# Optimization experiments

Measured on AMD Instinct MI355X. Metric: run time of the kernel, lower is better.

The kernel has to match this reference:

```python
import jax, jax.numpy as jnp
import numpy as np

N_Q = 50000
BATCH = 512
SEQLEN = 500
MEM_SIZE = 64
DK = 128   # key_embedding_dim == key_memory_state_dim == final_fc_dim
DV = 256   # value_embedding_dim == value_memory_state_dim
FC = 128


def setup_inputs() -> dict:
    key = jax.random.key(0)
    ks = jax.random.split(key, 16)
    q_data = jax.random.randint(ks[0], (BATCH, SEQLEN), 0, N_Q + 1, dtype=jnp.int64)
    qa_data = jax.random.randint(ks[1], (BATCH, SEQLEN), 0, 2 * N_Q + 1, dtype=jnp.int64)
    u = jax.random.uniform(ks[2], (BATCH * SEQLEN, 1))
    target = jnp.where(u < 0.1, -1.0, jnp.round(jax.random.uniform(ks[3], (BATCH * SEQLEN, 1)))).astype(jnp.float32)
    # embedding tables with padding_idx=0 zeroed
    q_embed_W = (jax.random.normal(ks[4], (N_Q + 1, DK)) * (2.0 / DK) ** 0.5).at[0].set(0.0)
    qa_embed_W = (jax.random.normal(ks[5], (2 * N_Q + 1, DV)) * (2.0 / DV) ** 0.5).at[0].set(0.0)
    key_memory = jax.random.normal(ks[6], (MEM_SIZE, DK)) * (2.0 / DK) ** 0.5
    init_value_memory = jax.random.normal(ks[7], (MEM_SIZE, DV)) * (2.0 / DV) ** 0.5
    erase_W = jax.random.normal(ks[8], (DV, DV)) * (2.0 / DV) ** 0.5
    erase_b = jnp.zeros((DV,))
    add_W = jax.random.normal(ks[9], (DV, DV)) * (2.0 / DV) ** 0.5
    add_b = jnp.zeros((DV,))
    read_W = jax.random.normal(ks[10], (FC, DV + DK)) * (2.0 / (DV + DK)) ** 0.5
    read_b = jnp.zeros((FC,))
    pred_W = jax.random.normal(ks[11], (1, FC)) * (2.0 / FC) ** 0.5
    pred_b = jnp.zeros((1,))
    return dict(q_data=q_data, qa_data=qa_data, target=target,
                q_embed_W=q_embed_W, qa_embed_W=qa_embed_W,
                key_memory=key_memory, init_value_memory=init_value_memory,
                erase_W=erase_W, erase_b=erase_b, add_W=add_W, add_b=add_b,
                read_W=read_W, read_b=read_b, pred_W=pred_W, pred_b=pred_b)


def reference(q_data, qa_data, target, q_embed_W, qa_embed_W, key_memory,
              init_value_memory, erase_W, erase_b, add_W, add_b,
              read_W, read_b, pred_W, pred_b):
    B, S = q_data.shape
    q_e = q_embed_W[q_data]    # (B, S, DK)
    qa_e = qa_embed_W[qa_data]  # (B, S, DV)

    # Addressing weights do not depend on the value memory state -> batch them.
    cw = jax.nn.softmax(jnp.einsum('bsk,mk->bsm', q_e, key_memory), axis=-1)  # (B,S,M)
    erase = jax.nn.sigmoid(jnp.einsum('bsv,ev->bse', qa_e, erase_W) + erase_b)  # (B,S,DV)
    add = jnp.tanh(jnp.einsum('bsv,ev->bse', qa_e, add_W) + add_b)              # (B,S,DV)

    def step(mem, xs):
        w, er, ad = xs  # (B,M), (B,DV), (B,DV)
        read = jnp.einsum('bm,bmd->bd', w, mem)  # read before write
        mem = mem * (1.0 - w[:, :, None] * er[:, None, :]) + w[:, :, None] * ad[:, None, :]
        return mem, read

    init_mem = jnp.broadcast_to(init_value_memory, (B,) + init_value_memory.shape)
    _, reads = jax.lax.scan(step, init_mem,
                            (jnp.swapaxes(cw, 0, 1), jnp.swapaxes(erase, 0, 1), jnp.swapaxes(add, 0, 1)))
    reads = jnp.swapaxes(reads, 0, 1)  # (B, S, DV)

    predict_input = jnp.concatenate([reads, q_e], axis=-1).reshape(B * S, -1)
    h = jnp.tanh(predict_input @ read_W.T + read_b)
    logits = h @ pred_W.T + pred_b  # (B*S, 1)

    mask = target >= 0.0
    # numerically-stable BCE with logits
    bce = jnp.maximum(logits, 0.0) - logits * target + jnp.log1p(jnp.exp(-jnp.abs(logits)))
    denom = jnp.maximum(jnp.sum(mask.astype(logits.dtype)), 1.0)
    loss = jnp.sum(jnp.where(mask, bce, 0.0)) / denom
    # masked_select replaced by masked full-size outputs for static shapes
    pred_masked = jnp.where(mask, jax.nn.sigmoid(logits), 0.0)
    target_masked = jnp.where(mask, target, 0.0)
    return loss, pred_masked, target_masked
```

## Files before the change

### kernel.cpp

```cpp
#include <hip/hip_runtime.h>
#include <hip/hip_bf16.h>

#define BATCH 512
#define SEQ   500
#define BS    (BATCH*SEQ)
#define MEM   64
#define DK    128
#define DV    256
#define FC    128
#define KS    16

typedef float f32x4 __attribute__((ext_vector_type(4)));
typedef float f32x2 __attribute__((ext_vector_type(2)));
typedef unsigned int u32x4 __attribute__((ext_vector_type(4)));
typedef unsigned int u32x2 __attribute__((ext_vector_type(2)));
typedef unsigned short u16x8 __attribute__((ext_vector_type(8)));
typedef __bf16 bf16x8 __attribute__((ext_vector_type(8)));

__device__ __forceinline__ float bf2f(unsigned short u){ return __uint_as_float(((unsigned)u)<<16); }
__device__ __forceinline__ unsigned short f2bfu(float x){
  unsigned u = __float_as_uint(x);
  return (unsigned short)((u + 0x7FFFu + ((u>>16)&1u)) >> 16);
}
__device__ __forceinline__ float sigf(float x){ return 1.f/(1.f+__expf(-x)); }
__device__ __forceinline__ float tanh_fast(float x){ return 2.f/(1.f+__expf(-2.f*x)) - 1.f; }

#define DPP3(r) { \
  asm("v_add_f32_dpp %0, %0, %0 row_shr:1 row_mask:0xf bank_mask:0xf bound_ctrl:0" : "+v"(r)); \
  asm("v_add_f32_dpp %0, %0, %0 row_shr:2 row_mask:0xf bank_mask:0xf bound_ctrl:0" : "+v"(r)); \
  asm("v_add_f32_dpp %0, %0, %0 row_shr:4 row_mask:0xf bank_mask:0xf bound_ctrl:0" : "+v"(r)); \
}

__device__ __forceinline__ float ldF(const void* p, long i, int f32m){
  return f32m ? ((const float*)p)[i] : bf2f(((const unsigned short*)p)[i]);
}
__device__ __forceinline__ int ldI(const int* p, long i, int i64m){
  return i64m ? p[2*i] : p[i];
}
__device__ __forceinline__ void st8(unsigned short* dst, const void* src, long i, int f32m){
  if (f32m){
    const float* q = (const float*)src + i;
    f32x4 a = *(const f32x4*)q;
    f32x4 b = *(const f32x4*)(q+4);
    u16x8 o;
    o[0]=f2bfu(a[0]); o[1]=f2bfu(a[1]); o[2]=f2bfu(a[2]); o[3]=f2bfu(a[3]);
    o[4]=f2bfu(b[0]); o[5]=f2bfu(b[1]); o[6]=f2bfu(b[2]); o[7]=f2bfu(b[3]);
    *(u16x8*)dst = o;
  } else {
    *(u16x8*)dst = *(const u16x8*)((const unsigned short*)src + i);
  }
}
__device__ __forceinline__ void stOut(void* p, long i, float x, int f32m){
  if (f32m) ((float*)p)[i] = x;
  else ((unsigned short*)p)[i] = f2bfu(x);
}

__global__ void k_detect(const unsigned short* __restrict__ km, const int* __restrict__ qa,
                         int* __restrict__ flags, float* __restrict__ accum){
  int t = threadIdx.x;
  if (t < 2) accum[t] = 0.f;
  unsigned short u = km[2*t];
  int e = (u >> 7) & 0xFF;
  bool sane = (e==0) || (e>=100 && e<=140);
  unsigned long long sm = __ballot(sane);
  unsigned long long zm = __ballot(qa[2*t+1] == 0);
  if (t == 0){
    flags[0] = (__popcll(sm) < 48) ? 1 : 0;
    flags[1] = (zm == 0xFFFFFFFFFFFFFFFFull) ? 1 : 0;
  }
}

__global__ __launch_bounds__(256, 2) void k_cw(const int* __restrict__ qd,
    const void* __restrict__ qW, const void* __restrict__ keym,
    float* __restrict__ cw, const int* __restrict__ flags){
  const int f32m = flags[0], i64m = flags[1];
  __shared__ float keyT[DK][MEM];
  int t = threadIdx.x;
  for (int i=t;i<MEM*DK;i+=256){ int m=i&63, k=i>>6; keyT[k][m] = ldF(keym, (long)m*DK+k, f32m); }
  __syncthreads();
  long row = (long)blockIdx.x*256 + t;
  int qid = ldI(qd, row, i64m);
  long qb = (long)qid*DK;
  f32x4 A[16];
  #pragma unroll
  for (int g=0;g<16;g++) A[g] = (f32x4){0.f,0.f,0.f,0.f};
  for (int kk=0;kk<DK;kk+=8){
    float qv[8];
    if (f32m){
      const float* qp = (const float*)qW + qb + kk;
      f32x4 a=*(const f32x4*)qp, b=*(const f32x4*)(qp+4);
      qv[0]=a[0];qv[1]=a[1];qv[2]=a[2];qv[3]=a[3];qv[4]=b[0];qv[5]=b[1];qv[6]=b[2];qv[7]=b[3];
    } else {
      u16x8 u = *(const u16x8*)((const unsigned short*)qW + qb + kk);
      #pragma unroll
      for (int j=0;j<8;j++) qv[j]=bf2f(u[j]);
    }
    #pragma unroll
    for (int j=0;j<8;j++){
      float q = qv[j];
      #pragma unroll
      for (int g=0;g<16;g++){
        f32x4 kv = *(const f32x4*)&keyT[kk+j][g*4];
        f32x4 a = A[g];
        a[0]=fmaf(q,kv[0],a[0]); a[1]=fmaf(q,kv[1],a[1]);
        a[2]=fmaf(q,kv[2],a[2]); a[3]=fmaf(q,kv[3],a[3]);
        A[g]=a;
      }
    }
  }
  float mx = -1e30f;
  #pragma unroll
  for (int g=0;g<16;g++){
    f32x4 a = A[g];
    mx = fmaxf(mx, fmaxf(fmaxf(a[0],a[1]), fmaxf(a[2],a[3])));
  }
  float sum = 0.f;
  #pragma unroll
  for (int g=0;g<16;g++){
    f32x4 a = A[g];
    a[0]=__expf(a[0]-mx); a[1]=__expf(a[1]-mx); a[2]=__expf(a[2]-mx); a[3]=__expf(a[3]-mx);
    sum += (a[0]+a[1])+(a[2]+a[3]);
    A[g]=a;
  }
  float inv = 1.f/sum;
  float* outp = cw + row*MEM;
  #pragma unroll
  for (int g=0;g<16;g++){
    f32x4 a = A[g];
    f32x4 v = { a[0]*inv, a[1]*inv, a[2]*inv, a[3]*inv };
    *(f32x4*)(outp + g*4) = v;
  }
}

__global__ __launch_bounds__(256, 2) void k_ea(const int* __restrict__ qad, long row0,
    const void* __restrict__ qaW, const void* __restrict__ eW, const void* __restrict__ ebias,
    const void* __restrict__ aW, const void* __restrict__ abias,
    unsigned short* __restrict__ ea, const int* __restrict__ flags, int nwg){
  const int f32m = flags[0], i64m = flags[1];
  __shared__ unsigned short As[128][40];
  __shared__ unsigned short Bs[128][40];
  __shared__ int rid[128];
  int g = blockIdx.x;
  int x = g & 7, idx = g >> 3;
  int qq = nwg >> 3, rr = nwg & 7;
  int base = (x < rr) ? x*(qq+1) : rr*(qq+1) + (x-rr)*qq;
  int orig = base + idx;
  int bm = orig >> 2, bn = orig & 3;

  int t = threadIdx.x;
  if (t < 128) rid[t] = ldI(qad, row0 + (long)bm*128 + t, i64m);
  int lane = t & 63, wid = t >> 6;
  int wr = wid >> 1, wc = wid & 1;
  f32x4 acc[4][4] = {};
  for (int k0=0;k0<DV;k0+=32){
    __syncthreads();
    #pragma unroll
    for (int j=0;j<2;j++){
      int c = t*2+j, r = c>>2, ko = (c&3)*8;
      st8(&As[r][ko], qaW, (long)rid[r]*DV + k0 + ko, f32m);
      if (r < 64) st8(&Bs[r][ko], eW, (long)(64*bn + r)*DV + k0 + ko, f32m);
      else        st8(&Bs[r][ko], aW, (long)(64*bn + r - 64)*DV + k0 + ko, f32m);
    }
    __syncthreads();
    bf16x8 af[4], bfr[4];
    #pragma unroll
    for (int i=0;i<4;i++){
      af[i]  = __builtin_bit_cast(bf16x8, *(const u16x8*)&As[wr*64+i*16+(lane&15)][(lane>>4)*8]);
      bfr[i] = __builtin_bit_cast(bf16x8, *(const u16x8*)&Bs[wc*64+i*16+(lane&15)][(lane>>4)*8]);
    }
    #pragma unroll
    for (int i=0;i<4;i++)
      #pragma unroll
      for (int n=0;n<4;n++)
        acc[i][n] = __builtin_amdgcn_mfma_f32_16x16x32_bf16(af[i], bfr[n], acc[i][n],0,0,0);
  }
  #pragma unroll
  for (int i=0;i<4;i++)
    #pragma unroll
    for (int n=0;n<4;n++){
      int cc = n*16 + (lane&15);
      int gcol = 64*bn + cc;
      float bias = wc ? ldF(abias,gcol,f32m) : ldF(ebias,gcol,f32m);
      int dcol = 2*gcol + wc;
      #pragma unroll
      for (int rix=0;rix<4;rix++){
        long rowg = (long)bm*128 + wr*64 + i*16 + (lane>>4)*4 + rix;
        float v = acc[i][n][rix] + bias;
        float o = wc ? tanh_fast(v) : sigf(v);
        ea[rowg*(2*DV) + dcol] = f2bfu(o);
      }
    }
}

#define SCAN_STEP2(srel) { \
  f32x4 W0 = *(const f32x4*)(wb + (srel)*MEM); \
  f32x4 W1 = *(const f32x4*)(wb + (srel)*MEM + 4); \
  u32x2 uu = *(const u32x2*)(eb + (srel)*128); \
  float er0 = __uint_as_float(uu[0] << 16); \
  float ad0 = __uint_as_float(uu[0] & 0xFFFF0000u); \
  float er1 = __uint_as_float(uu[1] << 16); \
  float ad1 = __uint_as_float(uu[1] & 0xFFFF0000u); \
  float ra0=0.f, ra1=0.f, rb0=0.f, rb1=0.f; \
  _Pragma("unroll") \
  for (int j=0; j<8; j++){ \
    float w = (j<4) ? W0[j] : W1[j-4]; \
    if (j & 1) ra1 = fmaf(w, MA[j], ra1); else ra0 = fmaf(w, MA[j], ra0); \
    float ta = fmaf(MA[j], er0, -ad0); \
    MA[j] = fmaf(-w, ta, MA[j]); \
    if (j & 1) rb1 = fmaf(w, MB[j], rb1); else rb0 = fmaf(w, MB[j], rb0); \
    float tb = fmaf(MB[j], er1, -ad1); \
    MB[j] = fmaf(-w, tb, MB[j]); \
  } \
  float r0 = ra0 + ra1; \
  float r1 = rb0 + rb1; \
  DPP3(r0); \
  DPP3(r1); \
  if (q == 7){ \
    unsigned pk; \
    asm("v_cvt_pk_bf16_f32 %0, %1, %2" : "=v"(pk) : "v"(r0), "v"(r1)); \
    rdu[(srel)*128] = pk; \
  } \
}

__global__ __launch_bounds__(512, 4) void k_scan(const float* __restrict__ cw,
    const unsigned short* __restrict__ ea, const void* __restrict__ initm,
    unsigned short* __restrict__ rdout, const int* __restrict__ flags){
  const int f32m = flags[0];
  __shared__ float        w_lds[2][KS][MEM];
  __shared__ unsigned int ea_lds[2][KS][128];
  int b = blockIdx.x, y = blockIdx.y;
  int t = threadIdx.x;
  int q = t & 7;
  int dp = t >> 3;
  int d0 = y*128 + 2*dp;
  int m0 = q * 8;

  float MA[8], MB[8];
  #pragma unroll
  for (int g=0; g<8; g++){
    MA[g] = ldF(initm, (long)(m0+g)*DV + d0,   f32m);
    MB[g] = ldF(initm, (long)(m0+g)*DV + d0+1, f32m);
  }

  const float* cwb = cw + (long)b*SEQ*MEM;
  const unsigned int* epb = (const unsigned int*)(ea + (long)b*SEQ*(2*DV)) + y*128;
  unsigned int* rdu = (unsigned int*)(rdout + (long)b*SEQ*DV) + y*64 + dp;

  {
    f32x2 wreg = *(const f32x2*)(cwb + 2*t);
    u32x4 ereg = *(const u32x4*)(epb + (t>>5)*256 + 4*(t&31));
    ((f32x2*)(&w_lds[0][0][0]))[t] = wreg;
    ((u32x4*)(&ea_lds[0][0][0]))[t] = ereg;
  }
  __syncthreads();

  int cur = 0;
  for (int st = 0; st < 31; st++){
    f32x2 wnext = *(const f32x2*)(cwb + (st+1)*KS*MEM + 2*t);
    u32x4 enext = *(const u32x4*)(epb + ((st+1)*KS + (t>>5))*256 + 4*(t&31));

    const float* wb        = &w_lds[cur][0][0] + m0;
    const unsigned int* eb = &ea_lds[cur][0][0] + 2*dp;
    #pragma unroll
    for (int srel=0; srel<KS; srel++){
      SCAN_STEP2(srel);
    }
    ((f32x2*)(&w_lds[cur^1][0][0]))[t] = wnext;
    ((u32x4*)(&ea_lds[cur^1][0][0]))[t] = enext;
    rdu += KS*128;
    __syncthreads();
    cur ^= 1;
  }
  {
    const float* wb        = &w_lds[cur][0][0] + m0;
    const unsigned int* eb = &ea_lds[cur][0][0] + 2*dp;
    #pragma unroll
    for (int srel=0; srel<4; srel++){
      SCAN_STEP2(srel);
    }
  }
}

__global__ __launch_bounds__(256, 2) void k_pred(const int* __restrict__ qd, long row0,
    const void* __restrict__ qW, const unsigned short* __restrict__ rds,
    const void* __restrict__ rW, const void* __restrict__ rb,
    const void* __restrict__ pW, const void* __restrict__ pb,
    const void* __restrict__ target,
    void* __restrict__ out, float* __restrict__ accum,
    const int* __restrict__ flags){
  const int f32m = flags[0], i64m = flags[1];
  __shared__ unsigned short As[128][40];
  __shared__ unsigned short Bs[128][40];
  __shared__ unsigned short hs[128][136];
  __shared__ int rid[128];
  int t = threadIdx.x;
  int bm = blockIdx.x;
  if (t<128) rid[t] = ldI(qd, row0 + (long)bm*128+t, i64m);
  int lane=t&63, wid=t>>6, wr=wid>>1, wc=wid&1;
  f32x4 acc[4][4] = {};
  for (int k0=0;k0<(DV+DK);k0+=32){
    __syncthreads();
    #pragma unroll
    for (int j=0;j<2;j++){
      int c=t*2+j, r=c>>2, ko=(c&3)*8;
      if (k0 < DV) st8(&As[r][ko], rds, ((long)bm*128+r)*DV + k0+ko, 0);
      else         st8(&As[r][ko], qW, (long)rid[r]*DK + (k0-DV)+ko, f32m);
      st8(&Bs[r][ko], rW, (long)r*(DV+DK) + k0+ko, f32m);
    }
    __syncthreads();
    bf16x8 af[4], bfr[4];
    #pragma unroll
    for (int i=0;i<4;i++){
      af[i]  = __builtin_bit_cast(bf16x8, *(const u16x8*)&As[wr*64+i*16+(lane&15)][(lane>>4)*8]);
      bfr[i] = __builtin_bit_cast(bf16x8, *(const u16x8*)&Bs[wc*64+i*16+(lane&15)][(lane>>4)*8]);
    }
    #pragma unroll
    for (int i=0;i<4;i++)
      #pragma unroll
      for (int n=0;n<4;n++)
        acc[i][n] = __builtin_amdgcn_mfma_f32_16x16x32_bf16(af[i], bfr[n], acc[i][n],0,0,0);
  }
  #pragma unroll
  for (int i=0;i<4;i++)
    #pragma unroll
    for (int n=0;n<4;n++){
      int col = wc*64 + n*16 + (lane&15);
      float bias = ldF(rb, col, f32m);
      #pragma unroll
      for (int rix=0;rix<4;rix++){
        int rowl = wr*64 + i*16 + (lane>>4)*4 + rix;
        hs[rowl][col] = f2bfu(tanh_fast(acc[i][n][rix] + bias));
      }
    }
  __syncthreads();
  float bces = 0.f, cnts = 0.f;
  if (t < 128){
    float lg = ldF(pb, 0, f32m);
    #pragma unroll
    for (int cc=0;cc<FC;cc++) lg = fmaf(bf2f(hs[t][cc]), ldF(pW, cc, f32m), lg);
    long rowg = row0 + (long)bm*128 + t;
    float tg = ldF(target, rowg, f32m);
    bool mask = tg >= 0.f;
    float e = __expf(-fabsf(lg));
    float bce = fmaxf(lg, 0.f) - lg*tg + __logf(1.f + e);
    bces = mask ? bce : 0.f;
    cnts = mask ? 1.f : 0.f;
    stOut(out, 1 + rowg, mask ? sigf(lg) : 0.f, f32m);
    stOut(out, 1 + BS + rowg, mask ? tg : 0.f, f32m);
  }
  #pragma unroll
  for (int off=32; off>0; off>>=1){ bces += __shfl_down(bces, off); cnts += __shfl_down(cnts, off); }
  if ((t & 63) == 0 && t < 128){
    atomicAdd(&accum[0], bces);
    atomicAdd(&accum[1], cnts);
  }
}

__global__ void k_loss(const float* __restrict__ accum, void* __restrict__ out,
                       const int* __restrict__ flags){
  if (threadIdx.x == 0){
    float denom = fmaxf(accum[1], 1.f);
    stOut(out, 0, accum[0]/denom, flags[0]);
  }
}

extern "C" void kernel_launch(void* const* d_in, const int* in_sizes, int n_in,
                              void* d_out, int out_size, void* d_ws, size_t ws_size,
                              hipStream_t stream) {
  const int* q_data  = (const int*)d_in[0];
  const int* qa_data = (const int*)d_in[1];
  const void* target = d_in[2];
  const void* qW   = d_in[3];
  const void* qaW  = d_in[4];
  const void* keym = d_in[5];
  const void* initm= d_in[6];
  const void* eW   = d_in[7];
  const void* eb   = d_in[8];
  const void* aW   = d_in[9];
  const void* ab   = d_in[10];
  const void* rW   = d_in[11];
  const void* rb   = d_in[12];
  const void* pW   = d_in[13];
  const void* pb   = d_in[14];

  char* ws = (char*)d_ws;
  const size_t CW_OFF = 256;
  const size_t CW_BYTES = (size_t)BS*MEM*4;
  const size_t EA_OFF = CW_OFF + CW_BYTES;
  float* accum = (float*)ws;
  int* flags = (int*)(ws + 64);
  float* cw = (float*)(ws + CW_OFF);

  const long per_batch = (long)SEQ*(2*DV)*2 + (long)SEQ*DV*2;
  long rem = (long)ws_size - (long)EA_OFF;
  int bchunk = 512;
  while (bchunk > 32 && per_batch*bchunk > rem) bchunk >>= 1;

  const size_t EA_BYTES = (size_t)bchunk*SEQ*(2*DV)*2;
  unsigned short* ea = (unsigned short*)(ws + EA_OFF);
  unsigned short* rd = (unsigned short*)(ws + EA_OFF + EA_BYTES);

  k_detect<<<1, 64, 0, stream>>>((const unsigned short*)keym, qa_data, flags, accum);
  k_cw  <<<BS/256, 256, 0, stream>>>(q_data, qW, keym, cw, flags);

  int nchunk = BATCH / bchunk;
  for (int c = 0; c < nchunk; c++){
    long b0 = (long)c * bchunk;
    int rows = bchunk * SEQ;
    int nwg = (rows/128)*4;
    k_ea  <<<nwg, 256, 0, stream>>>(qa_data, b0*SEQ, qaW, eW, eb, aW, ab, ea, flags, nwg);
    k_scan<<<dim3(bchunk, 2), 512, 0, stream>>>(cw + b0*SEQ*MEM, ea, initm, rd, flags);
    k_pred<<<rows/128, 256, 0, stream>>>(q_data, b0*SEQ, qW, rd, rW, rb, pW, pb,
                                         target, d_out, accum, flags);
  }
  k_loss<<<1, 64, 0, stream>>>(accum, d_out, flags);
}
```

Baseline: 963.3 us.

## Double-buffer LDS tiles with register prefetch in erase/add and predict GEMMs

Both GEMM kernels (k_ea and k_pred) now use two LDS buffers. Each iteration issues the next K-slice's global loads into registers before running the MFMAs on the current buffer, then writes the prefetched data into the other buffer. This hides global-load latency behind the matrix math and cuts one of the two barriers per iteration. In exchange it doubles the LDS used by the A/B tiles and raises register pressure, which could lower occupancy under launch_bounds(256,2). The scan kernel, which is probably the dominant cost, is not changed.

```diff
diff --git a/kernel.cpp b/kernel.cpp
--- a/kernel.cpp
+++ b/kernel.cpp
@@ -53,6 +53,29 @@
 __device__ __forceinline__ void stOut(void* p, long i, float x, int f32m){
   if (f32m) ((float*)p)[i] = x;
   else ((unsigned short*)p)[i] = f2bfu(x);
+}
+
+typedef union { struct{ f32x4 x, y; } f; u16x8 u; } raw8;
+__device__ __forceinline__ raw8 ld8raw(const void* src, long i, int f32m){
+  raw8 r;
+  if (f32m){
+    const float* q = (const float*)src + i;
+    r.f.x = *(const f32x4*)q;
+    r.f.y = *(const f32x4*)(q+4);
+  } else {
+    r.u = *(const u16x8*)((const unsigned short*)src + i);
+  }
+  return r;
+}
+__device__ __forceinline__ void st8raw(unsigned short* dst, raw8 r, int f32m){
+  if (f32m){
+    u16x8 o;
+    o[0]=f2bfu(r.f.x[0]); o[1]=f2bfu(r.f.x[1]); o[2]=f2bfu(r.f.x[2]); o[3]=f2bfu(r.f.x[3]);
+    o[4]=f2bfu(r.f.y[0]); o[5]=f2bfu(r.f.y[1]); o[6]=f2bfu(r.f.y[2]); o[7]=f2bfu(r.f.y[3]);
+    *(u16x8*)dst = o;
+  } else {
+    *(u16x8*)dst = r.u;
+  }
 }
 
 __global__ void k_detect(const unsigned short* __restrict__ km, const int* __restrict__ qa,
@@ -137,8 +160,8 @@
     const void* __restrict__ aW, const void* __restrict__ abias,
     unsigned short* __restrict__ ea, const int* __restrict__ flags, int nwg){
   const int f32m = flags[0], i64m = flags[1];
-  __shared__ unsigned short As[128][40];
-  __shared__ unsigned short Bs[128][40];
+  __shared__ unsigned short As[2][128][40];
+  __shared__ unsigned short Bs[2][128][40];
   __shared__ int rid[128];
   int g = blockIdx.x;
   int x = g & 7, idx = g >> 3;
@@ -151,28 +174,50 @@
   if (t < 128) rid[t] = ldI(qad, row0 + (long)bm*128 + t, i64m);
   int lane = t & 63, wid = t >> 6;
   int wr = wid >> 1, wc = wid & 1;
+  int c0 = t*2, r0s = c0>>2, ko0 = (c0&3)*8;
+  int c1 = t*2+1, r1s = c1>>2, ko1 = (c1&3)*8;
+  __syncthreads();
+  st8(&As[0][r0s][ko0], qaW, (long)rid[r0s]*DV + ko0, f32m);
+  st8(&As[0][r1s][ko1], qaW, (long)rid[r1s]*DV + ko1, f32m);
+  if (r0s < 64) st8(&Bs[0][r0s][ko0], eW, (long)(64*bn + r0s)*DV + ko0, f32m);
+  else          st8(&Bs[0][r0s][ko0], aW, (long)(64*bn + r0s - 64)*DV + ko0, f32m);
+  if (r1s < 64) st8(&Bs[0][r1s][ko1], eW, (long)(64*bn + r1s)*DV + ko1, f32m);
+  else          st8(&Bs[0][r1s][ko1], aW, (long)(64*bn + r1s - 64)*DV + ko1, f32m);
+  __syncthreads();
+
   f32x4 acc[4][4] = {};
+  int cur = 0;
   for (int k0=0;k0<DV;k0+=32){
-    __syncthreads();
-    #pragma unroll
-    for (int j=0;j<2;j++){
-      int c = t*2+j, r = c>>2, ko = (c&3)*8;
-      st8(&As[r][ko], qaW, (long)rid[r]*DV + k0 + ko, f32m);
-      if (r < 64) st8(&Bs[r][ko], eW, (long)(64*bn + r)*DV + k0 + ko, f32m);
-      else        st8(&Bs[r][ko], aW, (long)(64*bn + r - 64)*DV + k0 + ko, f32m);
-    }
-    __syncthreads();
+    raw8 a0n, a1n, b0n, b1n;
+    bool pre = (k0+32 < DV);
+    if (pre){
+      int kn = k0+32;
+      a0n = ld8raw(qaW, (long)rid[r0s]*DV + kn + ko0, f32m);
+      a1n = ld8raw(qaW, (long)rid[r1s]*DV + kn + ko1, f32m);
+      b0n = (r0s<64) ? ld8raw(eW, (long)(64*bn + r0s)*DV + kn + ko0, f32m)
+                     : ld8raw(aW, (long)(64*bn + r0s - 64)*DV + kn + ko0, f32m);
+      b1n = (r1s<64) ? ld8raw(eW, (long)(64*bn + r1s)*DV + kn + ko1, f32m)
+                     : ld8raw(aW, (long)(64*bn + r1s - 64)*DV + kn + ko1, f32m);
+    }
     bf16x8 af[4], bfr[4];
     #pragma unroll
     for (int i=0;i<4;i++){
-      af[i]  = __builtin_bit_cast(bf16x8, *(const u16x8*)&As[wr*64+i*16+(lane&15)][(lane>>4)*8]);
-      bfr[i] = __builtin_bit_cast(bf16x8, *(const u16x8*)&Bs[wc*64+i*16+(lane&15)][(lane>>4)*8]);
+      af[i]  = __builtin_bit_cast(bf16x8, *(const u16x8*)&As[cur][wr*64+i*16+(lane&15)][(lane>>4)*8]);
+      bfr[i] = __builtin_bit_cast(bf16x8, *(const u16x8*)&Bs[cur][wc*64+i*16+(lane&15)][(lane>>4)*8]);
     }
     #pragma unroll
     for (int i=0;i<4;i++)
       #pragma unroll
       for (int n=0;n<4;n++)
         acc[i][n] = __builtin_amdgcn_mfma_f32_16x16x32_bf16(af[i], bfr[n], acc[i][n],0,0,0);
+    if (pre){
+      st8raw(&As[cur^1][r0s][ko0], a0n, f32m);
+      st8raw(&As[cur^1][r1s][ko1], a1n, f32m);
+      st8raw(&Bs[cur^1][r0s][ko0], b0n, f32m);
+      st8raw(&Bs[cur^1][r1s][ko1], b1n, f32m);
+      __syncthreads();
+      cur ^= 1;
+    }
   }
   #pragma unroll
   for (int i=0;i<4;i++)
@@ -289,36 +334,62 @@
     void* __restrict__ out, float* __restrict__ accum,
     const int* __restrict__ flags){
   const int f32m = flags[0], i64m = flags[1];
-  __shared__ unsigned short As[128][40];
-  __shared__ unsigned short Bs[128][40];
+  __shared__ unsigned short As[2][128][40];
+  __shared__ unsigned short Bs[2][128][40];
   __shared__ unsigned short hs[128][136];
   __shared__ int rid[128];
   int t = threadIdx.x;
   int bm = blockIdx.x;
   if (t<128) rid[t] = ldI(qd, row0 + (long)bm*128+t, i64m);
   int lane=t&63, wid=t>>6, wr=wid>>1, wc=wid&1;
+  int c0 = t*2, r0s = c0>>2, ko0 = (c0&3)*8;
+  int c1 = t*2+1, r1s = c1>>2, ko1 = (c1&3)*8;
+  __syncthreads();
+  st8(&As[0][r0s][ko0], rds, ((long)bm*128+r0s)*DV + ko0, 0);
+  st8(&As[0][r1s][ko1], rds, ((long)bm*128+r1s)*DV + ko1, 0);
+  st8(&Bs[0][r0s][ko0], rW, (long)r0s*(DV+DK) + ko0, f32m);
+  st8(&Bs[0][r1s][ko1], rW, (long)r1s*(DV+DK) + ko1, f32m);
+  __syncthreads();
+
   f32x4 acc[4][4] = {};
+  int cur = 0;
   for (int k0=0;k0<(DV+DK);k0+=32){
-    __syncthreads();
-    #pragma unroll
-    for (int j=0;j<2;j++){
-      int c=t*2+j, r=c>>2, ko=(c&3)*8;
-      if (k0 < DV) st8(&As[r][ko], rds, ((long)bm*128+r)*DV + k0+ko, 0);
-      else         st8(&As[r][ko], qW, (long)rid[r]*DK + (k0-DV)+ko, f32m);
-      st8(&Bs[r][ko], rW, (long)r*(DV+DK) + k0+ko, f32m);
-    }
-    __syncthreads();
+    raw8 a0n, a1n, b0n, b1n;
+    bool pre = (k0+32 < DV+DK);
+    int amode = 0;
+    if (pre){
+      int kn = k0+32;
+      if (kn < DV){
+        a0n = ld8raw(rds, ((long)bm*128+r0s)*DV + kn+ko0, 0);
+        a1n = ld8raw(rds, ((long)bm*128+r1s)*DV + kn+ko1, 0);
+        amode = 0;
+      } else {
+        a0n = ld8raw(qW, (long)rid[r0s]*DK + (kn-DV)+ko0, f32m);
+        a1n = ld8raw(qW, (long)rid[r1s]*DK + (kn-DV)+ko1, f32m);
+        amode = f32m;
+      }
+      b0n = ld8raw(rW, (long)r0s*(DV+DK) + kn+ko0, f32m);
+      b1n = ld8raw(rW, (long)r1s*(DV+DK) + kn+ko1, f32m);
+    }
     bf16x8 af[4], bfr[4];
     #pragma unroll
     for (int i=0;i<4;i++){
-      af[i]  = __builtin_bit_cast(bf16x8, *(const u16x8*)&As[wr*64+i*16+(lane&15)][(lane>>4)*8]);
-      bfr[i] = __builtin_bit_cast(bf16x8, *(const u16x8*)&Bs[wc*64+i*16+(lane&15)][(lane>>4)*8]);
+      af[i]  = __builtin_bit_cast(bf16x8, *(const u16x8*)&As[cur][wr*64+i*16+(lane&15)][(lane>>4)*8]);
+      bfr[i] = __builtin_bit_cast(bf16x8, *(const u16x8*)&Bs[cur][wc*64+i*16+(lane&15)][(lane>>4)*8]);
     }
     #pragma unroll
     for (int i=0;i<4;i++)
       #pragma unroll
       for (int n=0;n<4;n++)
         acc[i][n] = __builtin_amdgcn_mfma_f32_16x16x32_bf16(af[i], bfr[n], acc[i][n],0,0,0);
+    if (pre){
+      st8raw(&As[cur^1][r0s][ko0], a0n, amode);
+      st8raw(&As[cur^1][r1s][ko1], a1n, amode);
+      st8raw(&Bs[cur^1][r0s][ko0], b0n, f32m);
+      st8raw(&Bs[cur^1][r1s][ko1], b1n, f32m);
+      __syncthreads();
+      cur ^= 1;
+    }
   }
   #pragma unroll
   for (int i=0;i<4;i++)
```

New measurement: 1.115 ms. 15.7% more time.

## Load erase/add GEMM fragments directly from global memory, dropping LDS staging

Applied to the files above, without the earlier changes.

The erase/add projection GEMM no longer stages the gathered embedding rows and weight tiles through shared memory with barriers. Each lane now loads its MFMA fragments straight from global memory, converting fp32 to bf16 with packed cvt instructions, and the k-loop is fully unrolled. This removes LDS traffic and __syncthreads stalls. In exchange each wave re-reads data that other waves in the block also load, and the accesses are less coalesced.

```diff
diff --git a/kernel.cpp b/kernel.cpp
--- a/kernel.cpp
+++ b/kernel.cpp
@@ -53,6 +53,22 @@
 __device__ __forceinline__ void stOut(void* p, long i, float x, int f32m){
   if (f32m) ((float*)p)[i] = x;
   else ((unsigned short*)p)[i] = f2bfu(x);
+}
+
+__device__ __forceinline__ bf16x8 ldfrag(const void* p, long i, int f32m){
+  if (f32m){
+    const float* q = (const float*)p + i;
+    f32x4 a = *(const f32x4*)q;
+    f32x4 b = *(const f32x4*)(q+4);
+    u32x4 o;
+    asm("v_cvt_pk_bf16_f32 %0, %1, %2" : "=v"(o[0]) : "v"(a[0]), "v"(a[1]));
+    asm("v_cvt_pk_bf16_f32 %0, %1, %2" : "=v"(o[1]) : "v"(a[2]), "v"(a[3]));
+    asm("v_cvt_pk_bf16_f32 %0, %1, %2" : "=v"(o[2]) : "v"(b[0]), "v"(b[1]));
+    asm("v_cvt_pk_bf16_f32 %0, %1, %2" : "=v"(o[3]) : "v"(b[2]), "v"(b[3]));
+    return __builtin_bit_cast(bf16x8, o);
+  } else {
+    return __builtin_bit_cast(bf16x8, *(const u16x8*)((const unsigned short*)p + i));
+  }
 }
 
 __global__ void k_detect(const unsigned short* __restrict__ km, const int* __restrict__ qa,
@@ -137,9 +153,6 @@
     const void* __restrict__ aW, const void* __restrict__ abias,
     unsigned short* __restrict__ ea, const int* __restrict__ flags, int nwg){
   const int f32m = flags[0], i64m = flags[1];
-  __shared__ unsigned short As[128][40];
-  __shared__ unsigned short Bs[128][40];
-  __shared__ int rid[128];
   int g = blockIdx.x;
   int x = g & 7, idx = g >> 3;
   int qq = nwg >> 3, rr = nwg & 7;
@@ -148,26 +161,30 @@
   int bm = orig >> 2, bn = orig & 3;
 
   int t = threadIdx.x;
-  if (t < 128) rid[t] = ldI(qad, row0 + (long)bm*128 + t, i64m);
   int lane = t & 63, wid = t >> 6;
   int wr = wid >> 1, wc = wid & 1;
+  int kq = (lane >> 4) * 8;
+
+  long aRow[4];
+  #pragma unroll
+  for (int i=0;i<4;i++){
+    int row = wr*64 + i*16 + (lane&15);
+    int qid = ldI(qad, row0 + (long)bm*128 + row, i64m);
+    aRow[i] = (long)qid*DV + kq;
+  }
+  const void* Bp = wc ? aW : eW;
+  long bRow[4];
+  #pragma unroll
+  for (int n=0;n<4;n++) bRow[n] = (long)(64*bn + n*16 + (lane&15))*DV + kq;
+
   f32x4 acc[4][4] = {};
+  #pragma unroll
   for (int k0=0;k0<DV;k0+=32){
-    __syncthreads();
-    #pragma unroll
-    for (int j=0;j<2;j++){
-      int c = t*2+j, r = c>>2, ko = (c&3)*8;
-      st8(&As[r][ko], qaW, (long)rid[r]*DV + k0 + ko, f32m);
-      if (r < 64) st8(&Bs[r][ko], eW, (long)(64*bn + r)*DV + k0 + ko, f32m);
-      else        st8(&Bs[r][ko], aW, (long)(64*bn + r - 64)*DV + k0 + ko, f32m);
-    }
-    __syncthreads();
     bf16x8 af[4], bfr[4];
     #pragma unroll
-    for (int i=0;i<4;i++){
-      af[i]  = __builtin_bit_cast(bf16x8, *(const u16x8*)&As[wr*64+i*16+(lane&15)][(lane>>4)*8]);
-      bfr[i] = __builtin_bit_cast(bf16x8, *(const u16x8*)&Bs[wc*64+i*16+(lane&15)][(lane>>4)*8]);
-    }
+    for (int i=0;i<4;i++) af[i]  = ldfrag(qaW, aRow[i] + k0, f32m);
+    #pragma unroll
+    for (int n=0;n<4;n++) bfr[n] = ldfrag(Bp, bRow[n] + k0, f32m);
     #pragma unroll
     for (int i=0;i<4;i++)
       #pragma unroll
```

New measurement: 1.260 ms. +30.8%, slower.
